# Performance work log

Measured on AMD Instinct MI355X. Metric: run time of the kernel, lower is better.

## Reference

```python
import jax, jax.numpy as jnp
import numpy as np

WIN_SIZE = 11
SIGMA = 1.5
WEIGHTS = np.array([0.0448, 0.2856, 0.3001, 0.2363, 0.1333], dtype=np.float32)
K1, K2 = 0.01, 0.03
DATA_RANGE = 255.0
C1 = (K1 * DATA_RANGE) ** 2
C2 = (K2 * DATA_RANGE) ** 2
N_SCALES = 5


def _gauss1d():
    coords = np.arange(WIN_SIZE, dtype=np.float32) - WIN_SIZE // 2
    g = np.exp(-(coords ** 2) / (2.0 * SIGMA ** 2))
    g /= g.sum()
    return jnp.asarray(g, dtype=jnp.float32)


def _blur(x, g):
    # separable depthwise gaussian blur, VALID padding (matches pytorch_msssim)
    C = x.shape[1]
    wh = jnp.tile(g.reshape(1, 1, 1, WIN_SIZE), (C, 1, 1, 1))
    wv = jnp.tile(g.reshape(1, 1, WIN_SIZE, 1), (C, 1, 1, 1))
    dn = ('NCHW', 'OIHW', 'NCHW')
    x = jax.lax.conv_general_dilated(x, wh, (1, 1), 'VALID', dimension_numbers=dn, feature_group_count=C)
    x = jax.lax.conv_general_dilated(x, wv, (1, 1), 'VALID', dimension_numbers=dn, feature_group_count=C)
    return x


def _ssim(X, Y, g):
    mu1 = _blur(X, g)
    mu2 = _blur(Y, g)
    mu1_sq = mu1 * mu1
    mu2_sq = mu2 * mu2
    mu1_mu2 = mu1 * mu2
    sigma1_sq = _blur(X * X, g) - mu1_sq
    sigma2_sq = _blur(Y * Y, g) - mu2_sq
    sigma12 = _blur(X * Y, g) - mu1_mu2
    cs_map = (2.0 * sigma12 + C2) / (sigma1_sq + sigma2_sq + C2)
    ssim_map = ((2.0 * mu1_mu2 + C1) / (mu1_sq + mu2_sq + C1)) * cs_map
    return ssim_map.mean(axis=(2, 3)), cs_map.mean(axis=(2, 3))  # [B,C] each


def _avg_pool2(x):
    # avg_pool2d kernel=2 stride=2; H,W chosen even at every scale so padding=0
    return jax.lax.reduce_window(x, 0.0, jax.lax.add, (1, 1, 2, 2), (1, 1, 2, 2), 'VALID') / 4.0


def setup_inputs() -> dict:
    key = jax.random.key(0)
    k1, k2 = jax.random.split(key)
    shape = (32, 3, 384, 384)
    prediction = jax.random.uniform(k1, shape, dtype=jnp.float32) * DATA_RANGE
    truth = jax.random.uniform(k2, shape, dtype=jnp.float32) * DATA_RANGE
    return {"prediction": prediction, "truth": truth}


def reference(prediction, truth):
    g = _gauss1d()
    w = jnp.asarray(WEIGHTS)
    X, Y = prediction, truth
    mcs = []
    for i in range(N_SCALES):
        ssim_pc, cs = _ssim(X, Y, g)
        if i < N_SCALES - 1:
            mcs.append(jax.nn.relu(cs))
            X = _avg_pool2(X)
            Y = _avg_pool2(Y)
    vals = jnp.stack(mcs + [jax.nn.relu(ssim_pc)], axis=0)  # [5,B,C]
    ms_ssim_val = jnp.prod(vals ** w.reshape(-1, 1, 1), axis=0)  # [B,C]
    return 1.0 - ms_ssim_val.mean()
```

## Files before the change

### kernel.cpp

```cpp
#include <hip/hip_runtime.h>
#include <math.h>


namespace {

constexpr int NIMG = 96;
constexpr float TWO_C1 = 13.005f;
constexpr float TWO_C2 = 117.045f;

__device__ constexpr float GW[11] = {
    0.00102838f, 0.00759875f, 0.03600077f, 0.10936070f, 0.21300553f,
    0.26601172f,
    0.21300553f, 0.10936070f, 0.03600077f, 0.00759875f, 0.00102838f};

typedef float f2 __attribute__((ext_vector_type(2)));

__device__ __forceinline__ f2 pk_mul(f2 a, f2 b) {
  f2 d;
  asm("v_pk_mul_f32 %0, %1, %2" : "=v"(d) : "v"(a), "v"(b));
  return d;
}
__device__ __forceinline__ f2 pk_mul_s1lo(f2 a, f2 b) {
  f2 d;
  asm("v_pk_mul_f32 %0, %1, %2 op_sel:[0,0] op_sel_hi:[1,0]"
      : "=v"(d) : "v"(a), "v"(b));
  return d;
}
__device__ __forceinline__ void fma_w(f2& d, f2 q, f2 p) {
  asm("v_pk_fma_f32 %0, %1, %2, %0 op_sel:[0,0,0] op_sel_hi:[0,1,1]"
      : "+v"(d) : "v"(q), "v"(p));
}
__device__ __forceinline__ void fma_nl(f2& d, f2 q, f2 t) {
  asm("v_pk_fma_f32 %0, %1, %2, %0 op_sel:[0,0,0] op_sel_hi:[1,0,1]"
      : "+v"(d) : "v"(q), "v"(t));
}
__device__ __forceinline__ void fma_nh(f2& d, f2 q, f2 t) {
  asm("v_pk_fma_f32 %0, %1, %2, %0 op_sel:[0,1,0] op_sel_hi:[1,1,1]"
      : "+v"(d) : "v"(q), "v"(t));
}
__device__ __forceinline__ void fma_sl(f2& d, f2 q, f2 t) {
  asm("v_pk_fma_f32 %0, %1, %2, %0 op_sel:[1,0,0] op_sel_hi:[0,0,1]"
      : "+v"(d) : "v"(q), "v"(t));
}
__device__ __forceinline__ void fma_sh(f2& d, f2 q, f2 t) {
  asm("v_pk_fma_f32 %0, %1, %2, %0 op_sel:[1,1,0] op_sel_hi:[0,1,1]"
      : "+v"(d) : "v"(q), "v"(t));
}

__device__ __forceinline__ float wshl1(float v) {
  return __int_as_float(__builtin_amdgcn_mov_dpp(
      __float_as_int(v), 0x130, 0xF, 0xF, true));
}
__device__ __forceinline__ f2 wshl1v(f2 v) {
  f2 r;
  r.x = wshl1(v.x);
  r.y = wshl1(v.y);
  return r;
}

struct SPtrs {
  const float* x[5];
  const float* y[5];
};

template <bool BASE, bool CLAMP>
__device__ __forceinline__ void vblur(const f2* __restrict__ PA,
                                      const f2* __restrict__ PB, int row0,
                                      int W2, int H, int cp, f2 (&AU)[4],
                                      f2 (&AW)[4], f2 (&BU)[4], f2 (&BW)[4],
                                      const f2 (&QQ)[6]) {
#pragma unroll
  for (int j = 0; j < 14; ++j) {
    int rin = row0 + j;
    if (CLAMP) rin = rin < H - 1 ? rin : H - 1;
    f2 pa = PA[(size_t)rin * W2 + cp];
    f2 pb = PB[(size_t)rin * W2 + cp];
    f2 Pu, Pw;
    if (BASE) { Pu = pa + pb; Pw = pa - pb; }
    else      { Pu = pa;      Pw = pb;      }
    f2 Qu = pk_mul(Pu, Pu), Qw = pk_mul(Pw, Pw);
#pragma unroll
    for (int i = 0; i < 4; ++i) {
      const int k = j - i;
      if (k >= 0 && k <= 10) {
        const int qi = k <= 5 ? k : 10 - k;
        fma_w(AU[i], QQ[qi], Pu);
        fma_w(AW[i], QQ[qi], Pw);
        fma_w(BU[i], QQ[qi], Qu);
        fma_w(BW[i], QQ[qi], Qw);
      }
    }
  }
}

__global__ __launch_bounds__(256, 6) void ssim_all(SPtrs sp,
                                                   float* __restrict__ acc) {
  __shared__ float red[2][4];

  const int tile = blockIdx.x;
  int s;
  if (tile < 96) s = 0;
  else if (tile < 120) s = 1;
  else if (tile < 126) s = 2;
  else if (tile < 129) s = 3;
  else s = 4;
  const int tstart[5] = {0, 96, 120, 126, 129};
  const int HH[5] = {384, 192, 96, 48, 24};
  const int NTX[5] = {4, 2, 1, 1, 1};
  const int TWM[5] = {94, 92, 86, 38, 14};
  const int lt = tile - tstart[s];
  const int H = HH[s], W = H, OH = H - 10, OW = W - 10, W2 = W >> 1;
  const int tx = lt % NTX[s], by = lt / NTX[s];
  const int x0 = tx * TWM[s];
  const int tw = (TWM[s] < OW - x0) ? TWM[s] : OW - x0;
  const int img = blockIdx.z;
  const f2* PA = (const f2*)sp.x[s] + (size_t)img * H * W2;
  const f2* PB = (const f2*)sp.y[s] + (size_t)img * H * W2;

  const int t = threadIdx.x;
  const int lane = t & 63, wv = t >> 6;
  int cp = (x0 >> 1) + lane;
  cp = cp < W2 - 1 ? cp : W2 - 1;
  const int row0 = by * 16 + wv * 4;

  f2 QQ[6];
  QQ[0].x = GW[0]; QQ[0].y = 0.f;
#pragma unroll
  for (int n = 1; n < 6; ++n) { QQ[n].x = GW[n]; QQ[n].y = GW[n - 1]; }

  float ssim_s = 0.f, cs_s = 0.f;

  if (row0 < OH) {
    f2 AU[4] = {}, AW[4] = {}, BU[4] = {}, BW[4] = {};
    const bool noclamp = (row0 + 13 <= H - 1);
    if (s == 0) {
      if (noclamp) vblur<true, false>(PA, PB, row0, W2, H, cp, AU, AW, BU, BW, QQ);
      else         vblur<true, true >(PA, PB, row0, W2, H, cp, AU, AW, BU, BW, QQ);
    } else {
      if (noclamp) vblur<false, false>(PA, PB, row0, W2, H, cp, AU, AW, BU, BW, QQ);
      else         vblur<false, true >(PA, PB, row0, W2, H, cp, AU, AW, BU, BW, QQ);
    }

    auto hb = [&QQ](f2 tt) -> f2 {
      f2 h = pk_mul_s1lo(QQ[0], tt);
      fma_nh(h, QQ[1], tt);
      tt = wshl1v(tt);
      fma_nl(h, QQ[2], tt);
      fma_nh(h, QQ[3], tt);
      tt = wshl1v(tt);
      fma_nl(h, QQ[4], tt);
      fma_nh(h, QQ[5], tt);
      tt = wshl1v(tt);
      fma_sl(h, QQ[5], tt);
      fma_sh(h, QQ[4], tt);
      tt = wshl1v(tt);
      fma_sl(h, QQ[3], tt);
      fma_sh(h, QQ[2], tt);
      tt = wshl1v(tt);
      fma_sl(h, QQ[1], tt);
      fma_sh(h, QQ[0], tt);
      return h;
    };

    const bool vx = (2 * lane) < tw;
    const bool vy = (2 * lane + 1) < tw;
#pragma unroll
    for (int i = 0; i < 4; ++i) {
      if (row0 + i < OH) {
        f2 bU = hb(AU[i]), bW = hb(AW[i]);
        f2 bU2 = hb(BU[i]), bW2 = hb(BW[i]);
        f2 m2u = pk_mul(bU, bU), m2w = pk_mul(bW, bW);
        f2 Pm = m2u - m2w;
        f2 Qm = m2u + m2w;
        f2 Am = bU2 - bW2;
        f2 Bm = bU2 + bW2;
        float csx = (Am.x - Pm.x + TWO_C2) *
                    __builtin_amdgcn_rcpf(Bm.x - Qm.x + TWO_C2);
        float lx = (Pm.x + TWO_C1) * __builtin_amdgcn_rcpf(Qm.x + TWO_C1);
        float csy = (Am.y - Pm.y + TWO_C2) *
                    __builtin_amdgcn_rcpf(Bm.y - Qm.y + TWO_C2);
        float ly = (Pm.y + TWO_C1) * __builtin_amdgcn_rcpf(Qm.y + TWO_C1);
        if (vx) { cs_s += csx; ssim_s += lx * csx; }
        if (vy) { cs_s += csy; ssim_s += ly * csy; }
      }
    }
  }

#pragma unroll
  for (int off = 32; off > 0; off >>= 1) {
    ssim_s += __shfl_down(ssim_s, off);
    cs_s += __shfl_down(cs_s, off);
  }
  if (lane == 0) { red[0][wv] = ssim_s; red[1][wv] = cs_s; }
  __syncthreads();
  if (t == 0) {
    atomicAdd(&acc[(2 * s + 0) * NIMG + img],
              red[0][0] + red[0][1] + red[0][2] + red[0][3]);
    atomicAdd(&acc[(2 * s + 1) * NIMG + img],
              red[1][0] + red[1][1] + red[1][2] + red[1][3]);
  }
}

__global__ __launch_bounds__(256) void pyramid_kernel(
    const float* __restrict__ X, const float* __restrict__ Y,
    float* __restrict__ u1, float* __restrict__ w1,
    float* __restrict__ u2, float* __restrict__ w2,
    float* __restrict__ u3, float* __restrict__ w3,
    float* __restrict__ u4, float* __restrict__ w4,
    float* __restrict__ acc) {
  const int img = blockIdx.y;
  const int t = threadIdx.x;
  if (blockIdx.x == 0 && img == 0) {
    for (int i = t; i < 10 * NIMG; i += 256) acc[i] = 0.f;
  }
  const int wv = t >> 6, lane = t & 63;
  const int tidx = blockIdx.x * 4 + wv;
  const int tx = tidx % 24, ty = tidx / 24;
  const int r = lane >> 3, c = lane & 7;

  const float* Xs = X + (size_t)img * 384 * 384;
  const float* Ys = Y + (size_t)img * 384 * 384;
  float* o1[2] = {u1 + (size_t)img * 192 * 192, w1 + (size_t)img * 192 * 192};
  float* o2[2] = {u2 + (size_t)img * 96 * 96,   w2 + (size_t)img * 96 * 96};
  float* o3[2] = {u3 + (size_t)img * 48 * 48,   w3 + (size_t)img * 48 * 48};
  float* o4[2] = {u4 + (size_t)img * 24 * 24,   w4 + (size_t)img * 24 * 24};

  int gr = ty * 16 + 2 * r, gc = tx * 16 + 2 * c;
  float2 xu = *(const float2*)&Xs[(size_t)gr * 384 + gc];
  float2 xv = *(const float2*)&Xs[(size_t)(gr + 1) * 384 + gc];
  float2 yu = *(const float2*)&Ys[(size_t)gr * 384 + gc];
  float2 yv = *(const float2*)&Ys[(size_t)(gr + 1) * 384 + gc];
  float l1x = 0.25f * (xu.x + xu.y + xv.x + xv.y);
  float l1y = 0.25f * (yu.x + yu.y + yv.x + yv.y);
  float lv[2] = {l1x + l1y, l1x - l1y};

#pragma unroll
  for (int ch = 0; ch < 2; ++ch) {
    float l1 = lv[ch];
    o1[ch][(size_t)(ty * 8 + r) * 192 + tx * 8 + c] = l1;

    float l2 = l1 + __shfl_xor(l1, 1);
    l2 = 0.25f * (l2 + __shfl_xor(l2, 8));
    if ((r & 1) == 0 && (c & 1) == 0)
      o2[ch][(size_t)(ty * 4 + (r >> 1)) * 96 + tx * 4 + (c >> 1)] = l2;

    float l3 = l2 + __shfl_xor(l2, 2);
    l3 = 0.25f * (l3 + __shfl_xor(l3, 16));
    if ((r & 3) == 0 && (c & 3) == 0)
      o3[ch][(size_t)(ty * 2 + (r >> 2)) * 48 + tx * 2 + (c >> 2)] = l3;

    float l4 = l3 + __shfl_xor(l3, 4);
    l4 = 0.25f * (l4 + __shfl_xor(l4, 32));
    if (lane == 0) o4[ch][(size_t)ty * 24 + tx] = l4;
  }
}

__global__ void final_kernel(const float* __restrict__ acc,
                             float* __restrict__ out) {
  __shared__ float prods[NIMG];
  const float wts[5] = {0.0448f, 0.2856f, 0.3001f, 0.2363f, 0.1333f};
  const float inv_npix[5] = {1.f / (374.f * 374.f), 1.f / (182.f * 182.f),
                             1.f / (86.f * 86.f),  1.f / (38.f * 38.f),
                             1.f / (14.f * 14.f)};
  int t = threadIdx.x;
  if (t < NIMG) {
    float p = 1.f;
#pragma unroll
    for (int s = 0; s < 5; ++s) {
      float sum = (s < 4) ? acc[(s * 2 + 1) * NIMG + t]
                          : acc[(s * 2 + 0) * NIMG + t];
      float m = sum * inv_npix[s];
      m = m > 0.f ? m : 0.f;
      p *= powf(m, wts[s]);
    }
    prods[t] = p;
  }
  __syncthreads();
  if (t == 0) {
    float s = 0.f;
    for (int i = 0; i < NIMG; ++i) s += prods[i];
    out[0] = 1.f - s / (float)NIMG;
  }
}

}

extern "C" void kernel_launch(void* const* d_in, const int* in_sizes, int n_in,
                              void* d_out, int out_size, void* d_ws,
                              size_t ws_size, hipStream_t stream) {
  const float* X0 = (const float*)d_in[0];
  const float* Y0 = (const float*)d_in[1];
  float* out = (float*)d_out;
  float* ws = (float*)d_ws;

  const size_t L1 = (size_t)NIMG * 192 * 192;
  const size_t L2 = (size_t)NIMG * 96 * 96;
  const size_t L3 = (size_t)NIMG * 48 * 48;
  const size_t L4 = (size_t)NIMG * 24 * 24;

  float* u1 = ws;
  float* u2 = u1 + L1;
  float* u3 = u2 + L2;
  float* u4 = u3 + L3;
  float* w1 = u4 + L4;
  float* w2 = w1 + L1;
  float* w3 = w2 + L2;
  float* w4 = w3 + L3;
  float* acc = w4 + L4;

  pyramid_kernel<<<dim3(144, NIMG), dim3(256), 0, stream>>>(
      X0, Y0, u1, w1, u2, w2, u3, w3, u4, w4, acc);

  SPtrs sp;
  sp.x[0] = X0; sp.x[1] = u1; sp.x[2] = u2; sp.x[3] = u3; sp.x[4] = u4;
  sp.y[0] = Y0; sp.y[1] = w1; sp.y[2] = w2; sp.y[3] = w3; sp.y[4] = w4;

  ssim_all<<<dim3(130, 1, NIMG), dim3(256), 0, stream>>>(sp, acc);

  final_kernel<<<dim3(1), dim3(128), 0, stream>>>(acc, out);
}
```

Before: 255.6 us.

## Interleave pyramid u/w planes and software-pipeline vertical blur row loads

```diff
diff --git a/kernel.cpp b/kernel.cpp
--- a/kernel.cpp
+++ b/kernel.cpp
@@ -14,6 +14,7 @@
     0.21300553f, 0.10936070f, 0.03600077f, 0.00759875f, 0.00102838f};
 
 typedef float f2 __attribute__((ext_vector_type(2)));
+typedef float f4 __attribute__((ext_vector_type(4)));
 
 __device__ __forceinline__ f2 pk_mul(f2 a, f2 b) {
   f2 d;
@@ -59,25 +60,55 @@
 }
 
 struct SPtrs {
-  const float* x[5];
-  const float* y[5];
+  const float* x0;
+  const float* y0;
+  const float* ip[4];
 };
 
 template <bool BASE, bool CLAMP>
-__device__ __forceinline__ void vblur(const f2* __restrict__ PA,
-                                      const f2* __restrict__ PB, int row0,
+__device__ __forceinline__ void vblur(const float* __restrict__ XP,
+                                      const float* __restrict__ YP, int row0,
                                       int W2, int H, int cp, f2 (&AU)[4],
                                       f2 (&AW)[4], f2 (&BU)[4], f2 (&BW)[4],
                                       const f2 (&QQ)[6]) {
-#pragma unroll
-  for (int j = 0; j < 14; ++j) {
+  const f2* PA = (const f2*)XP;
+  const f2* PB = (const f2*)YP;
+  const f4* PV = (const f4*)XP;
+  f2 sa[4], sb[4];
+  f4 sv[4];
+#pragma unroll
+  for (int j = 0; j < 4; ++j) {
     int rin = row0 + j;
     if (CLAMP) rin = rin < H - 1 ? rin : H - 1;
-    f2 pa = PA[(size_t)rin * W2 + cp];
-    f2 pb = PB[(size_t)rin * W2 + cp];
+    if (BASE) {
+      sa[j] = PA[(size_t)rin * W2 + cp];
+      sb[j] = PB[(size_t)rin * W2 + cp];
+    } else {
+      sv[j] = PV[(size_t)rin * W2 + cp];
+    }
+  }
+#pragma unroll
+  for (int j = 0; j < 14; ++j) {
     f2 Pu, Pw;
-    if (BASE) { Pu = pa + pb; Pw = pa - pb; }
-    else      { Pu = pa;      Pw = pb;      }
+    if (BASE) {
+      f2 pa = sa[j & 3], pb = sb[j & 3];
+      Pu = pa + pb;
+      Pw = pa - pb;
+    } else {
+      f4 v = sv[j & 3];
+      Pu.x = v.x; Pu.y = v.y;
+      Pw.x = v.z; Pw.y = v.w;
+    }
+    if (j + 4 < 14) {
+      int rin = row0 + j + 4;
+      if (CLAMP) rin = rin < H - 1 ? rin : H - 1;
+      if (BASE) {
+        sa[j & 3] = PA[(size_t)rin * W2 + cp];
+        sb[j & 3] = PB[(size_t)rin * W2 + cp];
+      } else {
+        sv[j & 3] = PV[(size_t)rin * W2 + cp];
+      }
+    }
     f2 Qu = pk_mul(Pu, Pu), Qw = pk_mul(Pw, Pw);
 #pragma unroll
     for (int i = 0; i < 4; ++i) {
@@ -93,7 +124,7 @@
   }
 }
 
-__global__ __launch_bounds__(256, 6) void ssim_all(SPtrs sp,
+__global__ __launch_bounds__(256, 5) void ssim_all(SPtrs sp,
                                                    float* __restrict__ acc) {
   __shared__ float red[2][4];
 
@@ -114,8 +145,15 @@
   const int x0 = tx * TWM[s];
   const int tw = (TWM[s] < OW - x0) ? TWM[s] : OW - x0;
   const int img = blockIdx.z;
-  const f2* PA = (const f2*)sp.x[s] + (size_t)img * H * W2;
-  const f2* PB = (const f2*)sp.y[s] + (size_t)img * H * W2;
+
+  const float* XP;
+  const float* YP = nullptr;
+  if (s == 0) {
+    XP = sp.x0 + (size_t)img * 384 * 384;
+    YP = sp.y0 + (size_t)img * 384 * 384;
+  } else {
+    XP = sp.ip[s - 1] + (size_t)img * H * W * 2;
+  }
 
   const int t = threadIdx.x;
   const int lane = t & 63, wv = t >> 6;
@@ -134,11 +172,11 @@
     f2 AU[4] = {}, AW[4] = {}, BU[4] = {}, BW[4] = {};
     const bool noclamp = (row0 + 13 <= H - 1);
     if (s == 0) {
-      if (noclamp) vblur<true, false>(PA, PB, row0, W2, H, cp, AU, AW, BU, BW, QQ);
-      else         vblur<true, true >(PA, PB, row0, W2, H, cp, AU, AW, BU, BW, QQ);
+      if (noclamp) vblur<true, false>(XP, YP, row0, W2, H, cp, AU, AW, BU, BW, QQ);
+      else         vblur<true, true >(XP, YP, row0, W2, H, cp, AU, AW, BU, BW, QQ);
     } else {
-      if (noclamp) vblur<false, false>(PA, PB, row0, W2, H, cp, AU, AW, BU, BW, QQ);
-      else         vblur<false, true >(PA, PB, row0, W2, H, cp, AU, AW, BU, BW, QQ);
+      if (noclamp) vblur<false, false>(XP, YP, row0, W2, H, cp, AU, AW, BU, BW, QQ);
+      else         vblur<false, true >(XP, YP, row0, W2, H, cp, AU, AW, BU, BW, QQ);
     }
 
     auto hb = [&QQ](f2 tt) -> f2 {
@@ -203,10 +241,8 @@
 
 __global__ __launch_bounds__(256) void pyramid_kernel(
     const float* __restrict__ X, const float* __restrict__ Y,
-    float* __restrict__ u1, float* __restrict__ w1,
-    float* __restrict__ u2, float* __restrict__ w2,
-    float* __restrict__ u3, float* __restrict__ w3,
-    float* __restrict__ u4, float* __restrict__ w4,
+    float* __restrict__ i1, float* __restrict__ i2,
+    float* __restrict__ i3, float* __restrict__ i4,
     float* __restrict__ acc) {
   const int img = blockIdx.y;
   const int t = threadIdx.x;
@@ -215,43 +251,63 @@
   }
   const int wv = t >> 6, lane = t & 63;
   const int tidx = blockIdx.x * 4 + wv;
-  const int tx = tidx % 24, ty = tidx / 24;
-  const int r = lane >> 3, c = lane & 7;
+  const int tx = tidx % 6, ty = tidx / 6;
+  const int r = lane >> 4, c = lane & 15;
 
   const float* Xs = X + (size_t)img * 384 * 384;
   const float* Ys = Y + (size_t)img * 384 * 384;
-  float* o1[2] = {u1 + (size_t)img * 192 * 192, w1 + (size_t)img * 192 * 192};
-  float* o2[2] = {u2 + (size_t)img * 96 * 96,   w2 + (size_t)img * 96 * 96};
-  float* o3[2] = {u3 + (size_t)img * 48 * 48,   w3 + (size_t)img * 48 * 48};
-  float* o4[2] = {u4 + (size_t)img * 24 * 24,   w4 + (size_t)img * 24 * 24};
-
-  int gr = ty * 16 + 2 * r, gc = tx * 16 + 2 * c;
-  float2 xu = *(const float2*)&Xs[(size_t)gr * 384 + gc];
-  float2 xv = *(const float2*)&Xs[(size_t)(gr + 1) * 384 + gc];
-  float2 yu = *(const float2*)&Ys[(size_t)gr * 384 + gc];
-  float2 yv = *(const float2*)&Ys[(size_t)(gr + 1) * 384 + gc];
-  float l1x = 0.25f * (xu.x + xu.y + xv.x + xv.y);
-  float l1y = 0.25f * (yu.x + yu.y + yv.x + yv.y);
-  float lv[2] = {l1x + l1y, l1x - l1y};
-
-#pragma unroll
-  for (int ch = 0; ch < 2; ++ch) {
-    float l1 = lv[ch];
-    o1[ch][(size_t)(ty * 8 + r) * 192 + tx * 8 + c] = l1;
-
-    float l2 = l1 + __shfl_xor(l1, 1);
-    l2 = 0.25f * (l2 + __shfl_xor(l2, 8));
-    if ((r & 1) == 0 && (c & 1) == 0)
-      o2[ch][(size_t)(ty * 4 + (r >> 1)) * 96 + tx * 4 + (c >> 1)] = l2;
-
-    float l3 = l2 + __shfl_xor(l2, 2);
-    l3 = 0.25f * (l3 + __shfl_xor(l3, 16));
-    if ((r & 3) == 0 && (c & 3) == 0)
-      o3[ch][(size_t)(ty * 2 + (r >> 2)) * 48 + tx * 2 + (c >> 2)] = l3;
-
-    float l4 = l3 + __shfl_xor(l3, 4);
-    l4 = 0.25f * (l4 + __shfl_xor(l4, 32));
-    if (lane == 0) o4[ch][(size_t)ty * 24 + tx] = l4;
+  f4* p1 = (f4*)i1 + (size_t)img * 192 * 96;
+  f4* p2 = (f4*)i2 + (size_t)img * 96 * 48;
+  f4* p3 = (f4*)i3 + (size_t)img * 48 * 24;
+  f4* p4 = (f4*)i4 + (size_t)img * 24 * 12;
+
+  float h4u = 0.f, h4w = 0.f;
+#pragma unroll
+  for (int b = 0; b < 2; ++b) {
+    const int gr = ty * 16 + b * 8 + 2 * r;
+    const int gc = tx * 64 + 4 * c;
+    f4 xu = *(const f4*)&Xs[(size_t)gr * 384 + gc];
+    f4 xv = *(const f4*)&Xs[(size_t)(gr + 1) * 384 + gc];
+    f4 yu = *(const f4*)&Ys[(size_t)gr * 384 + gc];
+    f4 yv = *(const f4*)&Ys[(size_t)(gr + 1) * 384 + gc];
+    float ax = 0.25f * (xu.x + xu.y + xv.x + xv.y);
+    float bx = 0.25f * (xu.z + xu.w + xv.z + xv.w);
+    float ay = 0.25f * (yu.x + yu.y + yv.x + yv.y);
+    float by = 0.25f * (yu.z + yu.w + yv.z + yv.w);
+    float u0 = ax + ay, u1v = bx + by, w0 = ax - ay, w1v = bx - by;
+    {
+      f4 st; st.x = u0; st.y = u1v; st.z = w0; st.w = w1v;
+      p1[(size_t)(ty * 8 + b * 4 + r) * 96 + tx * 16 + c] = st;
+    }
+    float hu = u0 + u1v, hw = w0 + w1v;
+    float su = 0.25f * (hu + __shfl_xor(hu, 16));
+    float sw = 0.25f * (hw + __shfl_xor(hw, 16));
+    float suh = __shfl_xor(su, 1), swh = __shfl_xor(sw, 1);
+    if ((r & 1) == 0 && (c & 1) == 0) {
+      f4 st; st.x = su; st.y = suh; st.z = sw; st.w = swh;
+      p2[(size_t)(ty * 4 + 2 * b + (r >> 1)) * 48 + tx * 8 + (c >> 1)] = st;
+    }
+    float au = su + __shfl_xor(su, 1);
+    float aw = sw + __shfl_xor(sw, 1);
+    float u3 = 0.25f * (au + __shfl_xor(au, 32));
+    float w3 = 0.25f * (aw + __shfl_xor(aw, 32));
+    float u3h = __shfl_xor(u3, 2), w3h = __shfl_xor(w3, 2);
+    if (r == 0 && (c & 3) == 0) {
+      f4 st; st.x = u3; st.y = u3h; st.z = w3; st.w = w3h;
+      p3[(size_t)(ty * 2 + b) * 24 + tx * 4 + (c >> 2)] = st;
+    }
+    float hu4 = u3 + __shfl_xor(u3, 2);
+    float hw4 = w3 + __shfl_xor(w3, 2);
+    if (b == 0) {
+      h4u = hu4; h4w = hw4;
+    } else {
+      float l4u = 0.25f * (h4u + hu4), l4w = 0.25f * (h4w + hw4);
+      float l4uh = __shfl_xor(l4u, 4), l4wh = __shfl_xor(l4w, 4);
+      if (r == 0 && (c & 7) == 0) {
+        f4 st; st.x = l4u; st.y = l4uh; st.z = l4w; st.w = l4wh;
+        p4[(size_t)ty * 12 + tx * 2 + (c >> 3)] = st;
+      }
+    }
   }
 }
 
@@ -293,27 +349,23 @@
   float* out = (float*)d_out;
   float* ws = (float*)d_ws;
 
-  const size_t L1 = (size_t)NIMG * 192 * 192;
-  const size_t L2 = (size_t)NIMG * 96 * 96;
-  const size_t L3 = (size_t)NIMG * 48 * 48;
-  const size_t L4 = (size_t)NIMG * 24 * 24;
-
-  float* u1 = ws;
-  float* u2 = u1 + L1;
-  float* u3 = u2 + L2;
-  float* u4 = u3 + L3;
-  float* w1 = u4 + L4;
-  float* w2 = w1 + L1;
-  float* w3 = w2 + L2;
-  float* w4 = w3 + L3;
-  float* acc = w4 + L4;
-
-  pyramid_kernel<<<dim3(144, NIMG), dim3(256), 0, stream>>>(
-      X0, Y0, u1, w1, u2, w2, u3, w3, u4, w4, acc);
+  const size_t L1 = (size_t)NIMG * 192 * 192 * 2;
+  const size_t L2 = (size_t)NIMG * 96 * 96 * 2;
+  const size_t L3 = (size_t)NIMG * 48 * 48 * 2;
+  const size_t L4 = (size_t)NIMG * 24 * 24 * 2;
+
+  float* i1 = ws;
+  float* i2 = i1 + L1;
+  float* i3 = i2 + L2;
+  float* i4 = i3 + L3;
+  float* acc = i4 + L4;
+
+  pyramid_kernel<<<dim3(36, NIMG), dim3(256), 0, stream>>>(
+      X0, Y0, i1, i2, i3, i4, acc);
 
   SPtrs sp;
-  sp.x[0] = X0; sp.x[1] = u1; sp.x[2] = u2; sp.x[3] = u3; sp.x[4] = u4;
-  sp.y[0] = Y0; sp.y[1] = w1; sp.y[2] = w2; sp.y[3] = w3; sp.y[4] = w4;
+  sp.x0 = X0; sp.y0 = Y0;
+  sp.ip[0] = i1; sp.ip[1] = i2; sp.ip[2] = i3; sp.ip[3] = i4;
 
   ssim_all<<<dim3(130, 1, NIMG), dim3(256), 0, stream>>>(sp, acc);
 
```

After: 241.0 us. 1.06x faster.
